# Kernel optimization log

Measured on AMD Instinct MI355X. Metric: run time of the kernel, lower is better.

## Reference

```python
import jax, jax.numpy as jnp
import numpy as np

START_TAG = 8
STOP_TAG = 9
NEG_INF = -10000.0


def setup_inputs() -> dict:
    key = jax.random.key(0)
    k1, k2, k3 = jax.random.split(key, 3)
    S, B, T = 2048, 4096, 10
    feats = jax.random.normal(k1, (S, B, T), dtype=jnp.float32)
    lengths = jax.random.randint(k2, (B,), 1, S + 1, dtype=jnp.int32)
    transitions = jax.random.normal(k3, (T, T), dtype=jnp.float32)
    # transitions[next, prev]; nothing transitions INTO start, nothing OUT of stop
    transitions = transitions.at[START_TAG, :].set(NEG_INF).at[:, STOP_TAG].set(NEG_INF)
    return {"feats": feats, "transitions": transitions, "lengths": lengths}


def reference(feats, transitions, lengths):
    # Viterbi decode (the module's forward).
    S, B, T = feats.shape
    bidx = jnp.arange(B)
    init = jnp.full((B, T), NEG_INF, feats.dtype).at[:, START_TAG].set(0.0)

    def step(fv, feat):
        # fv: [B, T_prev]; transitions: [T_next, T_prev]
        ntv = fv[:, None, :] + transitions[None, :, :]      # [B, Tn, Tp]
        best = jnp.argmax(ntv, axis=2).astype(jnp.int32)    # [B, Tn]
        fv_new = jnp.max(ntv, axis=2) + feat                # [B, Tn]
        return fv_new, (fv_new, best)

    _, (fv_steps, bptrs) = jax.lax.scan(step, init, feats)
    fv_all = jnp.concatenate([init[None], fv_steps], axis=0)  # [S+1, B, T]

    last_fv = fv_all[lengths, bidx, :]                       # [B, T]
    terminal = last_fv + transitions[STOP_TAG][None, :]
    path_score = jnp.max(terminal, axis=1)                   # [B]
    best_last = jnp.argmax(terminal, axis=1).astype(jnp.int32)

    # Vectorized backtrace over all batches, scanning time in reverse.
    def bt_step(cur, j):
        nxt_j = jnp.minimum(j + 1, S - 1)
        gathered = bptrs[nxt_j, bidx, cur]                   # [B]
        cur_new = jnp.where(j == lengths - 1, best_last,
                  jnp.where(j < lengths - 1, gathered, cur))
        path_j = jnp.where(j < lengths, cur_new, 0)
        return cur_new, path_j

    _, paths_rev = jax.lax.scan(bt_step, best_last, jnp.arange(S - 1, -1, -1))
    best_paths = paths_rev[::-1].T                           # [B, S]
    return path_score, best_paths
```

## Files before the change

kernel.cpp:

```cpp
#include <hip/hip_runtime.h>
#include <stdint.h>
#include <stddef.h>

#define S_LEN 2048
#define B_N   4096
#define T_N   10
#define NCH   128
#define NEG_INF_F (-10000.0f)

template<int CTRL>
__device__ __forceinline__ int dppi(int v) {
    return __builtin_amdgcn_update_dpp(0, v, CTRL, 0xF, 0xF, true);
}

static __device__ __forceinline__ int imin(int a, int b) { return a < b ? a : b; }
static __device__ __forceinline__ int imax(int a, int b) { return a > b ? a : b; }

static __device__ __forceinline__ float vmax3(float a, float b, float c) {
    float d;
    asm("v_max3_f32 %0, %1, %2, %3" : "=v"(d) : "v"(a), "v"(b), "v"(c));
    return d;
}

__global__ void __launch_bounds__(256) viterbi_fwd(const float* __restrict__ feats,
                                                   const float* __restrict__ trans,
                                                   const int* __restrict__ lengths,
                                                   float* __restrict__ ckpt) {
    const float FNINF = __int_as_float(0xff800000);
    const int tid = threadIdx.x;
    const int t   = tid & 15;
    const int b   = blockIdx.x * 16 + (tid >> 4);
    const bool act = (t < T_N);
    const int len = lengths[b];

    int lenW = len;
    lenW = imax(lenW, __shfl_xor(lenW, 16, 64));
    lenW = imax(lenW, __shfl_xor(lenW, 32, 64));
    lenW = __builtin_amdgcn_readfirstlane(lenW);

    int q[16];
    q[0]  = t;
    q[1]  = dppi<0x121>(t);  q[2]  = dppi<0x122>(t);  q[3]  = dppi<0x123>(t);
    q[4]  = dppi<0x124>(t);  q[5]  = dppi<0x125>(t);  q[6]  = dppi<0x126>(t);
    q[7]  = dppi<0x127>(t);  q[8]  = dppi<0x128>(t);  q[9]  = dppi<0x129>(t);
    q[10] = dppi<0x12A>(t);  q[11] = dppi<0x12B>(t);  q[12] = dppi<0x12C>(t);
    q[13] = dppi<0x12D>(t);  q[14] = dppi<0x12E>(t);  q[15] = dppi<0x12F>(t);

    float trr[16];
    #pragma unroll
    for (int r = 0; r < 16; ++r) {
        bool v = act && (q[r] < T_N);
        trr[r] = v ? trans[t * T_N + q[r]] : FNINF;
    }

    const float* fptr = feats + (size_t)b * T_N + imin(t, T_N - 1);
    auto ldfeat = [&](int s) -> float {
        return fptr[(size_t)imin(s, S_LEN - 1) * (B_N * T_N)];
    };

    float fvr;
    {
        float finit = (t == 8) ? 0.0f : NEG_INF_F;
        asm("v_mov_b32 %0, %1\n\ts_nop 1" : "=v"(fvr) : "v"(finit));
    }

    float bA[16], bB[16], bC[16];
    #pragma unroll
    for (int u = 0; u < 16; ++u) bA[u] = ldfeat(u);
    #pragma unroll
    for (int u = 0; u < 16; ++u) bB[u] = ldfeat(16 + u);
    #pragma unroll
    for (int u = 0; u < 16; ++u) bC[u] = ldfeat(32 + u);

    auto step16 = [&](float (&f)[16]) {
        #pragma unroll
        for (int u = 0; u < 16; ++u) {
            float cd[16];
            cd[0] = fvr + trr[0];
#define DPPADD(N, S) asm("v_add_f32_dpp %0, %1, %2 " S " row_mask:0xf bank_mask:0xf" \
                         : "=v"(cd[N]) : "v"(fvr), "v"(trr[N]))
            DPPADD(1,  "row_ror:1");  DPPADD(2,  "row_ror:2");  DPPADD(3,  "row_ror:3");
            DPPADD(4,  "row_ror:4");  DPPADD(5,  "row_ror:5");  DPPADD(6,  "row_ror:6");
            DPPADD(7,  "row_ror:7");  DPPADD(8,  "row_ror:8");  DPPADD(9,  "row_ror:9");
            DPPADD(10, "row_ror:10"); DPPADD(11, "row_ror:11"); DPPADD(12, "row_ror:12");
            DPPADD(13, "row_ror:13"); DPPADD(14, "row_ror:14"); DPPADD(15, "row_ror:15");
#undef DPPADD
            float x0 = vmax3(cd[0],  cd[1],  cd[2]);
            float x1 = vmax3(cd[3],  cd[4],  cd[5]);
            float x2 = vmax3(cd[6],  cd[7],  cd[8]);
            float x3 = vmax3(cd[9],  cd[10], cd[11]);
            float x4 = vmax3(cd[12], cd[13], cd[14]);
            float y0 = vmax3(x0, x1, x2);
            float y1 = vmax3(x3, x4, cd[15]);
            float mm = fmaxf(y0, y1);
            asm("v_add_f32 %0, %1, %2\n\ts_nop 1" : "=v"(fvr) : "v"(mm), "v"(f[u]));
        }
    };
    auto ckstore = [&](int snext) {
        if (act && snext <= len && snext <= S_LEN - 16)
            ckpt[((size_t)(snext >> 4) * B_N + b) * T_N + t] = fvr;
    };

    for (int s0 = 0; s0 < lenW; s0 += 48) {
        step16(bA); ckstore(s0 + 16);
        #pragma unroll
        for (int u = 0; u < 16; ++u) bA[u] = ldfeat(s0 + 48 + u);

        step16(bB); ckstore(s0 + 32);
        #pragma unroll
        for (int u = 0; u < 16; ++u) bB[u] = ldfeat(s0 + 64 + u);

        step16(bC); ckstore(s0 + 48);
        #pragma unroll
        for (int u = 0; u < 16; ++u) bC[u] = ldfeat(s0 + 80 + u);
    }
}

__global__ void __launch_bounds__(256) bt_maps(const float* __restrict__ feats,
                                               const float* __restrict__ trans,
                                               const int* __restrict__ lengths,
                                               const float* __restrict__ ckpt,
                                               unsigned* __restrict__ bpd,
                                               unsigned char* __restrict__ bpb,
                                               uint2* __restrict__ gmap,
                                               float* __restrict__ lastfv) {
    const int c = blockIdx.x >> 4;
    const int b = ((blockIdx.x & 15) << 8) + threadIdx.x;
    const int len = lengths[b];
    const int r0 = c * 16;
    const int kl = len - r0;

    if (kl < 0) {
        gmap[(size_t)c * B_N + b] = make_uint2(0x76543210u, 0x98u);
        return;
    }

    float fv[T_N];
    if (c == 0) {
        #pragma unroll
        for (int p = 0; p < T_N; ++p) fv[p] = (p == 8) ? 0.0f : NEG_INF_F;
    } else {
        #pragma unroll
        for (int p = 0; p < T_N; ++p) fv[p] = ckpt[((size_t)c * B_N + b) * T_N + p];
    }

    float* lfp = lastfv + (size_t)b * T_N;
    if (kl == 0) {
        #pragma unroll
        for (int n = 0; n < T_N; ++n) lfp[n] = fv[n];
        gmap[(size_t)c * B_N + b] = make_uint2(0x76543210u, 0x98u);
        return;
    }

    const float* frow = feats + ((size_t)r0 * B_N + b) * T_N;
    const size_t rstride = (size_t)B_N * T_N;

    float2 bufA[5], bufB[5];
    {
        const float2* p2 = (const float2*)frow;
        #pragma unroll
        for (int i = 0; i < 5; ++i) bufA[i] = p2[i];
    }

    unsigned Glo = 0x76543210u, Ghi = 0x98u;

    {
        if (r0 + 1 < len) {
            const float2* p2 = (const float2*)(frow + rstride);
            #pragma unroll
            for (int i = 0; i < 5; ++i) bufB[i] = p2[i];
        }
        float m[T_N];
        #pragma unroll
        for (int n = 0; n < T_N; ++n) {
            float cd[T_N];
            #pragma unroll
            for (int p = 0; p < T_N; ++p) cd[p] = fv[p] + trans[n * T_N + p];
            float x0 = vmax3(cd[0], cd[1], cd[2]);
            float x1 = vmax3(cd[3], cd[4], cd[5]);
            float x2 = vmax3(cd[6], cd[7], cd[8]);
            m[n] = fmaxf(vmax3(x0, x1, x2), cd[9]);
        }
        #pragma unroll
        for (int n = 0; n < T_N; ++n)
            fv[n] = m[n] + ((n & 1) ? bufA[n >> 1].y : bufA[n >> 1].x);
    }

    auto bodyM = [&](int k, float2 (&cur)[5], float2 (&nxt)[5], bool doPrefetch, bool doFv) {
        if (doPrefetch && (r0 + k + 1 < len)) {
            const float2* p2 = (const float2*)(frow + (size_t)(k + 1) * rstride);
            #pragma unroll
            for (int i = 0; i < 5; ++i) nxt[i] = p2[i];
        }
        if (k == kl) {
            #pragma unroll
            for (int n = 0; n < T_N; ++n) lfp[n] = fv[n];
        }
        unsigned mlo = 0, mhi = 0, nGlo = 0, nGhi = 0;
        unsigned long long G64 = ((unsigned long long)Ghi << 32) | Glo;
        float m[T_N];
        #pragma unroll
        for (int n = 0; n < T_N; ++n) {
            float cd[T_N];
            #pragma unroll
            for (int p = 0; p < T_N; ++p) cd[p] = fv[p] + trans[n * T_N + p];
            float x0 = vmax3(cd[0], cd[1], cd[2]);
            float x1 = vmax3(cd[3], cd[4], cd[5]);
            float x2 = vmax3(cd[6], cd[7], cd[8]);
            float mm = fmaxf(vmax3(x0, x1, x2), cd[9]);
            m[n] = mm;
            int ix = 9;
            #pragma unroll
            for (int p = 8; p >= 0; --p) ix = (cd[p] == mm) ? p : ix;
            unsigned nib = (unsigned)(G64 >> (ix << 2)) & 15u;
            if (n < 8) { mlo |= (unsigned)ix << (4 * n);       nGlo |= nib << (4 * n); }
            else       { mhi |= (unsigned)ix << (4 * (n - 8)); nGhi |= nib << (4 * (n - 8)); }
        }
        const int r = r0 + k;
        if (r < len) {
            bpd[(size_t)r * B_N + b] = mlo;
            bpb[(size_t)r * B_N + b] = (unsigned char)mhi;
            Glo = nGlo; Ghi = nGhi;
        }
        if (doFv) {
            #pragma unroll
            for (int n = 0; n < T_N; ++n)
                fv[n] = m[n] + ((n & 1) ? cur[n >> 1].y : cur[n >> 1].x);
        }
    };

    #pragma unroll 1
    for (int k = 1; k < 15; k += 2) {
        bodyM(k,     bufB, bufA, true,  true);
        bodyM(k + 1, bufA, bufB, true,  true);
    }
    bodyM(15, bufB, bufA, false, true);
    bodyM(16, bufA, bufB, false, false);

    gmap[(size_t)c * B_N + b] = make_uint2(Glo, Ghi);
}

static __device__ __forceinline__ int bpapply(uint2 w, int cur) {
    unsigned long long w64 = ((unsigned long long)w.y << 32) | (unsigned long long)w.x;
    return (int)((w64 >> (cur * 4)) & 15ULL);
}

__global__ void __launch_bounds__(256) bt_compose(const uint2* __restrict__ gmap,
                                                  const float* __restrict__ lastfv,
                                                  const float* __restrict__ trans,
                                                  unsigned char* __restrict__ entry,
                                                  float* __restrict__ score) {
    const int b = blockIdx.x * 256 + threadIdx.x;

    float term[T_N];
    #pragma unroll
    for (int n = 0; n < T_N; ++n)
        term[n] = lastfv[(size_t)b * T_N + n] + trans[9 * T_N + n];
    float x0 = vmax3(term[0], term[1], term[2]);
    float x1 = vmax3(term[3], term[4], term[5]);
    float x2 = vmax3(term[6], term[7], term[8]);
    float pm = fmaxf(vmax3(x0, x1, x2), term[9]);
    int st = 9;
    #pragma unroll
    for (int n = 8; n >= 0; --n) st = (term[n] == pm) ? n : st;
    score[b] = pm;

    uint2 wA[16], wB[16];
    auto pre = [&](uint2 (&W)[16], int cb) {
        #pragma unroll
        for (int u = 0; u < 16; ++u) W[u] = gmap[(size_t)(cb * 16 + u) * B_N + b];
    };
    auto proc = [&](uint2 (&W)[16], int cb) {
        #pragma unroll
        for (int u = 15; u >= 0; --u) {
            int cc = cb * 16 + u;
            entry[(size_t)cc * B_N + b] = (unsigned char)st;
            st = bpapply(W[u], st);
        }
    };
    pre(wA, 7);
    pre(wB, 6); proc(wA, 7);
    pre(wA, 5); proc(wB, 6);
    pre(wB, 4); proc(wA, 5);
    pre(wA, 3); proc(wB, 4);
    pre(wB, 2); proc(wA, 3);
    pre(wA, 1); proc(wB, 2);
    pre(wB, 0); proc(wA, 1);
    proc(wB, 0);
}

__global__ void __launch_bounds__(256) bt_emit(const unsigned* __restrict__ bpd,
                                               const unsigned char* __restrict__ bpb,
                                               const int* __restrict__ lengths,
                                               const unsigned char* __restrict__ entry,
                                               float* __restrict__ opaths) {
    const int c = blockIdx.x >> 4;
    const int b = ((blockIdx.x & 15) << 8) + threadIdx.x;
    const int len = lengths[b];
    const int r0 = c * 16 + 1;

    unsigned Wd[16], Wb[16];
    #pragma unroll
    for (int u = 0; u < 16; ++u) {
        int r = r0 + u;
        unsigned d = 0x76543210u, h = 0x98u;
        if (r < len) { d = bpd[(size_t)r * B_N + b]; h = bpb[(size_t)r * B_N + b]; }
        Wd[u] = d; Wb[u] = h;
    }

    int cur = entry[(size_t)c * B_N + b];
    float buf[16];
    #pragma unroll
    for (int u = 15; u >= 0; --u) {
        unsigned long long w = ((unsigned long long)Wb[u] << 32) | Wd[u];
        cur = (int)((w >> ((cur * 4) & 63)) & 15ULL);
        buf[u] = (c * 16 + u < len) ? (float)cur : 0.0f;
    }
    float* op = opaths + (size_t)b * S_LEN + c * 16;
    #pragma unroll
    for (int qq = 0; qq < 4; ++qq)
        *(float4*)(op + qq * 4) = make_float4(buf[qq*4+0], buf[qq*4+1], buf[qq*4+2], buf[qq*4+3]);
}

extern "C" void kernel_launch(void* const* d_in, const int* in_sizes, int n_in,
                              void* d_out, int out_size, void* d_ws, size_t ws_size,
                              hipStream_t stream) {
    const float* feats   = (const float*)d_in[0];
    const float* trans   = (const float*)d_in[1];
    const int*   lengths = (const int*)d_in[2];
    float* out = (float*)d_out;

    char* w = (char*)d_ws;
    float*         ckpt  = (float*)w;          w += (size_t)NCH * B_N * T_N * 4;
    unsigned*      bpd   = (unsigned*)w;       w += (size_t)(S_LEN + 1) * B_N * 4;
    unsigned char* bpb   = (unsigned char*)w;  w += (size_t)(S_LEN + 1) * B_N;
    uint2*         gmap  = (uint2*)w;          w += (size_t)NCH * B_N * 8;
    unsigned char* entry = (unsigned char*)w;  w += (size_t)NCH * B_N;
    float*         lastfv = (float*)w;

    viterbi_fwd<<<B_N / 16, 256, 0, stream>>>(feats, trans, lengths, ckpt);
    bt_maps   <<<NCH * (B_N / 256), 256, 0, stream>>>(feats, trans, lengths, ckpt, bpd, bpb, gmap, lastfv);
    bt_compose<<<B_N / 256, 256, 0, stream>>>(gmap, lastfv, trans, entry, out);
    bt_emit   <<<NCH * (B_N / 256), 256, 0, stream>>>(bpd, bpb, lengths, entry, out + B_N);
}
```

Before: 336.2 us.

## Shrink feature prefetch depth in forward and backtrace kernels, early-exit emit

The forward scan drops its triple 16-step feature buffers for a double 8-step buffer, loading the next 8 steps before computing the current 8, and stores a checkpoint every 16 steps. The backtrace-map kernel drops its ping-pong prefetch and loads each row's features right before it is used, inside a non-unrolled loop. The emit kernel now writes zeros and returns early for chunks past the sequence length. This lowers register pressure and possibly raises occupancy, but it hides much less load latency on the serial recurrence.

After: 338.3 us. No clear change (+0.6%).

```diff
diff --git a/kernel.cpp b/kernel.cpp
--- a/kernel.cpp
+++ b/kernel.cpp
@@ -64,17 +64,16 @@
         asm("v_mov_b32 %0, %1\n\ts_nop 1" : "=v"(fvr) : "v"(finit));
     }
 
-    float bA[16], bB[16], bC[16];
-    #pragma unroll
-    for (int u = 0; u < 16; ++u) bA[u] = ldfeat(u);
-    #pragma unroll
-    for (int u = 0; u < 16; ++u) bB[u] = ldfeat(16 + u);
-    #pragma unroll
-    for (int u = 0; u < 16; ++u) bC[u] = ldfeat(32 + u);
-
-    auto step16 = [&](float (&f)[16]) {
-        #pragma unroll
-        for (int u = 0; u < 16; ++u) {
+    float fA[8], fB[8];
+    #pragma unroll
+    for (int u = 0; u < 8; ++u) fA[u] = ldfeat(u);
+
+    for (int s0 = 0; s0 < lenW; s0 += 8) {
+        #pragma unroll
+        for (int u = 0; u < 8; ++u) fB[u] = ldfeat(s0 + 8 + u);
+
+        #pragma unroll
+        for (int u = 0; u < 8; ++u) {
             float cd[16];
             cd[0] = fvr + trr[0];
 #define DPPADD(N, S) asm("v_add_f32_dpp %0, %1, %2 " S " row_mask:0xf bank_mask:0xf" \
@@ -93,26 +92,16 @@
             float y0 = vmax3(x0, x1, x2);
             float y1 = vmax3(x3, x4, cd[15]);
             float mm = fmaxf(y0, y1);
-            asm("v_add_f32 %0, %1, %2\n\ts_nop 1" : "=v"(fvr) : "v"(mm), "v"(f[u]));
-        }
-    };
-    auto ckstore = [&](int snext) {
-        if (act && snext <= len && snext <= S_LEN - 16)
-            ckpt[((size_t)(snext >> 4) * B_N + b) * T_N + t] = fvr;
-    };
-
-    for (int s0 = 0; s0 < lenW; s0 += 48) {
-        step16(bA); ckstore(s0 + 16);
-        #pragma unroll
-        for (int u = 0; u < 16; ++u) bA[u] = ldfeat(s0 + 48 + u);
-
-        step16(bB); ckstore(s0 + 32);
-        #pragma unroll
-        for (int u = 0; u < 16; ++u) bB[u] = ldfeat(s0 + 64 + u);
-
-        step16(bC); ckstore(s0 + 48);
-        #pragma unroll
-        for (int u = 0; u < 16; ++u) bC[u] = ldfeat(s0 + 80 + u);
+            asm("v_add_f32 %0, %1, %2\n\ts_nop 1" : "=v"(fvr) : "v"(mm), "v"(fA[u]));
+        }
+
+        const int snext = s0 + 8;
+        if ((snext & 15) == 0) {
+            if (act && snext <= len && snext <= S_LEN - 16)
+                ckpt[((size_t)(snext >> 4) * B_N + b) * T_N + t] = fvr;
+        }
+        #pragma unroll
+        for (int u = 0; u < 8; ++u) fA[u] = fB[u];
     }
 }
 
@@ -152,24 +141,19 @@
         return;
     }
 
-    const float* frow = feats + ((size_t)r0 * B_N + b) * T_N;
     const size_t rstride = (size_t)B_N * T_N;
-
-    float2 bufA[5], bufB[5];
+    const float* fbase = feats + (size_t)b * T_N;
+
+    float buf[T_N];
     {
-        const float2* p2 = (const float2*)frow;
-        #pragma unroll
-        for (int i = 0; i < 5; ++i) bufA[i] = p2[i];
+        const float2* p2 = (const float2*)(fbase + (size_t)r0 * rstride);
+        #pragma unroll
+        for (int i = 0; i < 5; ++i) { float2 v = p2[i]; buf[2*i] = v.x; buf[2*i+1] = v.y; }
     }
 
     unsigned Glo = 0x76543210u, Ghi = 0x98u;
 
     {
-        if (r0 + 1 < len) {
-            const float2* p2 = (const float2*)(frow + rstride);
-            #pragma unroll
-            for (int i = 0; i < 5; ++i) bufB[i] = p2[i];
-        }
         float m[T_N];
         #pragma unroll
         for (int n = 0; n < T_N; ++n) {
@@ -182,15 +166,16 @@
             m[n] = fmaxf(vmax3(x0, x1, x2), cd[9]);
         }
         #pragma unroll
-        for (int n = 0; n < T_N; ++n)
-            fv[n] = m[n] + ((n & 1) ? bufA[n >> 1].y : bufA[n >> 1].x);
-    }
-
-    auto bodyM = [&](int k, float2 (&cur)[5], float2 (&nxt)[5], bool doPrefetch, bool doFv) {
-        if (doPrefetch && (r0 + k + 1 < len)) {
-            const float2* p2 = (const float2*)(frow + (size_t)(k + 1) * rstride);
-            #pragma unroll
-            for (int i = 0; i < 5; ++i) nxt[i] = p2[i];
+        for (int n = 0; n < T_N; ++n) fv[n] = m[n] + buf[n];
+    }
+
+    #pragma unroll 1
+    for (int k = 1; k <= 16; ++k) {
+        const int r = r0 + k;
+        {
+            const float2* p2 = (const float2*)(fbase + (size_t)imin(r, S_LEN - 1) * rstride);
+            #pragma unroll
+            for (int i = 0; i < 5; ++i) { float2 v = p2[i]; buf[2*i] = v.x; buf[2*i+1] = v.y; }
         }
         if (k == kl) {
             #pragma unroll
@@ -216,26 +201,16 @@
             if (n < 8) { mlo |= (unsigned)ix << (4 * n);       nGlo |= nib << (4 * n); }
             else       { mhi |= (unsigned)ix << (4 * (n - 8)); nGhi |= nib << (4 * (n - 8)); }
         }
-        const int r = r0 + k;
         if (r < len) {
             bpd[(size_t)r * B_N + b] = mlo;
             bpb[(size_t)r * B_N + b] = (unsigned char)mhi;
             Glo = nGlo; Ghi = nGhi;
         }
-        if (doFv) {
-            #pragma unroll
-            for (int n = 0; n < T_N; ++n)
-                fv[n] = m[n] + ((n & 1) ? cur[n >> 1].y : cur[n >> 1].x);
-        }
-    };
-
-    #pragma unroll 1
-    for (int k = 1; k < 15; k += 2) {
-        bodyM(k,     bufB, bufA, true,  true);
-        bodyM(k + 1, bufA, bufB, true,  true);
-    }
-    bodyM(15, bufB, bufA, false, true);
-    bodyM(16, bufA, bufB, false, false);
+        if (k < 16) {
+            #pragma unroll
+            for (int n = 0; n < T_N; ++n) fv[n] = m[n] + buf[n];
+        }
+    }
 
     gmap[(size_t)c * B_N + b] = make_uint2(Glo, Ghi);
 }
@@ -297,8 +272,16 @@
     const int c = blockIdx.x >> 4;
     const int b = ((blockIdx.x & 15) << 8) + threadIdx.x;
     const int len = lengths[b];
+    float* op = opaths + (size_t)b * S_LEN + c * 16;
+
+    if (c * 16 >= len) {
+        float4 z = make_float4(0.f, 0.f, 0.f, 0.f);
+        #pragma unroll
+        for (int qq = 0; qq < 4; ++qq) *(float4*)(op + qq * 4) = z;
+        return;
+    }
+
     const int r0 = c * 16 + 1;
-
     unsigned Wd[16], Wb[16];
     #pragma unroll
     for (int u = 0; u < 16; ++u) {
@@ -316,7 +299,6 @@
         cur = (int)((w >> ((cur * 4) & 63)) & 15ULL);
         buf[u] = (c * 16 + u < len) ? (float)cur : 0.0f;
     }
-    float* op = opaths + (size_t)b * S_LEN + c * 16;
     #pragma unroll
     for (int qq = 0; qq < 4; ++qq)
         *(float4*)(op + qq * 4) = make_float4(buf[qq*4+0], buf[qq*4+1], buf[qq*4+2], buf[qq*4+3]);
```
